# Kernel optimization log

Measured on AMD Instinct MI355X. Metric: run time of the kernel, lower is better.

## Reference

```python
import jax, jax.numpy as jnp
import numpy as np

N = 50000       # nodes
E = 800000      # edges (before self-loops)
G = 64          # graphs in batch
F_IN = 128      # node_features
HID = 64        # hidden_channels
H1 = 8          # conv1 heads
NEG_SLOPE = 0.2
EPS = 1e-16


def _gat_layer(x, src, dst, W, att_src, att_dst, bias, heads, out_ch, concat):
    """PyG GATConv (eval mode: dropout inactive). src/dst include self-loops.
    x: [N, F_in]; W: [F_in, heads*out_ch]; att_*: [heads, out_ch]; bias: [heads*out_ch] or [out_ch]."""
    n = x.shape[0]
    h = (x @ W).reshape(n, heads, out_ch)                 # [N,H,C]
    a_s = jnp.sum(h * att_src, axis=-1)                   # [N,H]
    a_d = jnp.sum(h * att_dst, axis=-1)                   # [N,H]
    e = jax.nn.leaky_relu(a_s[src] + a_d[dst], NEG_SLOPE)  # [Etot,H]
    # segment softmax over incoming edges of each destination node
    m = jax.ops.segment_max(e, dst, num_segments=n)       # [N,H]
    e = jnp.exp(e - m[dst])
    denom = jax.ops.segment_sum(e, dst, num_segments=n)   # [N,H]
    alpha = e / (denom[dst] + EPS)                        # [Etot,H]
    msg = h[src] * alpha[:, :, None]                      # [Etot,H,C]
    out = jax.ops.segment_sum(msg, dst, num_segments=n)   # [N,H,C]
    if concat:
        out = out.reshape(n, heads * out_ch)
    else:
        out = out.mean(axis=1)
    return out + bias


def setup_inputs() -> dict:
    key = jax.random.key(0)
    ks = jax.random.split(key, 14)
    x = jax.random.normal(ks[0], (N, F_IN), dtype=jnp.float32)
    edge_index = jax.random.randint(ks[1], (2, E), 0, N, dtype=jnp.int64)
    batch_index = jnp.sort(jax.random.randint(ks[2], (N,), 0, G, dtype=jnp.int64))
    s = 0.05
    return {
        "x": x,
        "edge_index": edge_index,
        "batch_index": batch_index,
        "W1": jax.random.normal(ks[3], (F_IN, H1 * HID), dtype=jnp.float32) * s,
        "att_src1": jax.random.normal(ks[4], (H1, HID), dtype=jnp.float32) * s,
        "att_dst1": jax.random.normal(ks[5], (H1, HID), dtype=jnp.float32) * s,
        "b1": jnp.zeros((H1 * HID,), dtype=jnp.float32),
        "W2": jax.random.normal(ks[6], (H1 * HID, HID), dtype=jnp.float32) * s,
        "att_src2": jax.random.normal(ks[7], (1, HID), dtype=jnp.float32) * s,
        "att_dst2": jax.random.normal(ks[8], (1, HID), dtype=jnp.float32) * s,
        "b2": jnp.zeros((HID,), dtype=jnp.float32),
        "lin_W": jax.random.normal(ks[9], (HID, 1), dtype=jnp.float32) * s,
        "lin_b": jnp.zeros((1,), dtype=jnp.float32),
    }


def reference(x, edge_index, batch_index, W1, att_src1, att_dst1, b1,
              W2, att_src2, att_dst2, b2, lin_W, lin_b):
    n = x.shape[0]
    loops = jnp.arange(n, dtype=edge_index.dtype)
    src = jnp.concatenate([edge_index[0], loops])
    dst = jnp.concatenate([edge_index[1], loops])
    # eval mode: F.dropout is identity
    h = jax.nn.elu(_gat_layer(x, src, dst, W1, att_src1, att_dst1, b1, H1, HID, True))
    h = _gat_layer(h, src, dst, W2, att_src2, att_dst2, b2, 1, HID, False)
    # global mean pool over graphs
    sums = jax.ops.segment_sum(h, batch_index, num_segments=G)          # [G,HID]
    cnt = jax.ops.segment_sum(jnp.ones((n,), h.dtype), batch_index, num_segments=G)
    pooled = sums / jnp.maximum(cnt, 1.0)[:, None]
    return pooled @ lin_W + lin_b                                       # [G,1]
```

## Files before the change

### kernel.cpp

```cpp
#include <hip/hip_runtime.h>
#include <math.h>

#define NN 50000
#define EE 800000
#define ET 850000
#define GG 64
#define MPAD 50048
#define NCAP 64
#define NROW 50016
#define CSRI (NROW * NCAP)
#define CSTRIDE 32

typedef __attribute__((ext_vector_type(8))) short bf16x8;
typedef __attribute__((ext_vector_type(4))) float f32x4;

__device__ __forceinline__ float lrelu(float v) { return v > 0.f ? v : 0.2f * v; }

__device__ __forceinline__ unsigned short f2bf(float f) {
  unsigned u = __float_as_uint(f);
  u += 0x7FFFu + ((u >> 16) & 1u);
  return (unsigned short)(u >> 16);
}
__device__ __forceinline__ unsigned pack2(float a, float b) {
  return (unsigned)f2bf(a) | ((unsigned)f2bf(b) << 16);
}
__device__ __forceinline__ void i8acc(uint2 u, float a, float* o) {
  o[0] += a * (float)((int)(u.x << 24) >> 24);
  o[1] += a * (float)((int)(u.x << 16) >> 24);
  o[2] += a * (float)((int)(u.x <<  8) >> 24);
  o[3] += a * (float)((int)u.x >> 24);
  o[4] += a * (float)((int)(u.y << 24) >> 24);
  o[5] += a * (float)((int)(u.y << 16) >> 24);
  o[6] += a * (float)((int)(u.y <<  8) >> 24);
  o[7] += a * (float)((int)u.y >> 24);
}

#define INIT_BLOCKS 1563
#define CVT_X_BLOCKS 3128
#define CVT_W_BLOCKS 256
#define V_BLOCKS 2
#define GSEG_BLOCKS 196
__global__ __launch_bounds__(256) void prep_kernel(const float* __restrict__ x,
                                                   const float* __restrict__ W1,
                                                   const float* __restrict__ W2,
                                                   const float* __restrict__ att_s2,
                                                   const float* __restrict__ att_d2,
                                                   const float* __restrict__ linW,
                                                   const int* __restrict__ batch,
                                                   unsigned short* __restrict__ xb,
                                                   unsigned short* __restrict__ W1T,
                                                   float* __restrict__ Vs,
                                                   float* __restrict__ Vd,
                                                   float* __restrict__ Vz,
                                                   int* __restrict__ gstart,
                                                   int* __restrict__ cursor,
                                                   unsigned short* __restrict__ csr) {
  int b = blockIdx.x;
  if (b < INIT_BLOCKS) {
    int i = b * 256 + threadIdx.x;
    if (i < CSRI / 8) {
      uint4 sf = {0xC350C350u, 0xC350C350u, 0xC350C350u, 0xC350C350u};
      ((uint4*)csr)[i] = sf;
    }
    if (i < NROW) cursor[i * CSTRIDE] = 0;
  } else if (b < INIT_BLOCKS + CVT_X_BLOCKS) {
    int i8 = (b - INIT_BLOCKS) * 256 + threadIdx.x;
    if (i8 >= MPAD * 128 / 8) return;
    size_t e0 = (size_t)i8 * 8;
    int row = (int)(e0 >> 7);
    uint4 o;
    if (row < NN) {
      float4 f0 = *(const float4*)(x + e0);
      float4 f1 = *(const float4*)(x + e0 + 4);
      o.x = pack2(f0.x, f0.y); o.y = pack2(f0.z, f0.w);
      o.z = pack2(f1.x, f1.y); o.w = pack2(f1.z, f1.w);
    } else {
      o.x = o.y = o.z = o.w = 0u;
    }
    *(uint4*)(xb + e0) = o;
  } else if (b < INIT_BLOCKS + CVT_X_BLOCKS + CVT_W_BLOCKS) {
    int i = (b - INIT_BLOCKS - CVT_X_BLOCKS) * 256 + threadIdx.x;
    int k = i >> 9, n = i & 511;
    W1T[n * 128 + k] = f2bf(W1[i]);
  } else if (b < INIT_BLOCKS + CVT_X_BLOCKS + CVT_W_BLOCKS + V_BLOCKS) {
    int k = (b - INIT_BLOCKS - CVT_X_BLOCKS - CVT_W_BLOCKS) * 256 + threadIdx.x;
    float vs = 0.f, vd = 0.f, vz = 0.f;
#pragma unroll 8
    for (int c = 0; c < 64; ++c) {
      float w = W2[k * 64 + c];
      vs += w * att_s2[c];
      vd += w * att_d2[c];
      vz += w * linW[c];
    }
    Vs[k] = vs; Vd[k] = vd; Vz[k] = vz;
  } else {
    int e = (b - INIT_BLOCKS - CVT_X_BLOCKS - CVT_W_BLOCKS - V_BLOCKS) * 256 + threadIdx.x;
    if (e < NN) {
      int bb = batch[e];
      if (e == 0) {
        for (int g = 0; g <= bb; ++g) gstart[g] = 0;
      } else {
        int pb = batch[e - 1];
        for (int g = pb + 1; g <= bb; ++g) gstart[g] = e;
      }
      if (e == NN - 1) {
        for (int g = bb + 1; g <= GG; ++g) gstart[g] = NN;
      }
    }
  }
}

#define GEMM_BLOCKS 3128
#define SCAT_BLOCKS 831
#define SCAT_STRIDE (SCAT_BLOCKS * 256)
__global__ __launch_bounds__(256) void gemm1_scatter(const unsigned short* __restrict__ xb,
                                                     const unsigned short* __restrict__ W1T,
                                                     const float* __restrict__ att_s,
                                                     const float* __restrict__ att_d,
                                                     unsigned char* __restrict__ h1i,
                                                     float2* __restrict__ asc,
                                                     float* __restrict__ ad1,
                                                     const int* __restrict__ ei,
                                                     int* __restrict__ cursor,
                                                     unsigned short* __restrict__ csr) {
  __shared__ unsigned char st8[2][64 * 72];
  const int idx = blockIdx.x;
  const bool is_scat = ((idx & 3) == 3) && ((idx >> 2) < SCAT_BLOCKS);
  if (is_scat) {
    int base = (idx >> 2) * 256 + threadIdx.x;
#pragma unroll
    for (int k = 0; k < 4; ++k) {
      int e = base + k * SCAT_STRIDE;
      if (e < ET) {
        int src = (e < EE) ? ei[e] : (e - EE);
        int dst = (e < EE) ? ei[EE + e] : (e - EE);
        int pos = atomicAdd(&cursor[dst * CSTRIDE], 1);
        if (pos < NCAP) csr[dst * NCAP + pos] = (unsigned short)src;
      }
    }
    return;
  }
  const int gi = idx - min((idx + 1) >> 2, SCAT_BLOCKS);

  const int t = threadIdx.x, w = t >> 6, l = t & 63;
  const int bm = (gi >> 2) * 64;
  const int ypair = gi & 3;
  const int m16 = l & 15, q = l >> 4;
  const int row = bm + w * 16 + m16;

  const bf16x8* Ap = (const bf16x8*)(xb + (size_t)row * 128 + q * 8);
  bf16x8 a0 = Ap[0], a1 = Ap[4], a2 = Ap[8], a3 = Ap[12];

  const int r2 = t >> 2, c16 = (t & 3) * 16;

#pragma unroll
  for (int hh = 0; hh < 2; ++hh) {
    const int h = ypair * 2 + hh;
    const bf16x8* Bp = (const bf16x8*)(W1T + (size_t)(h * 64 + m16) * 128 + q * 8);
    f32x4 acc[4] = {};
#pragma unroll
    for (int c = 0; c < 4; ++c) {
      acc[c] = __builtin_amdgcn_mfma_f32_16x16x32_bf16(a0, Bp[(size_t)c * 256 + 0],  acc[c], 0, 0, 0);
      acc[c] = __builtin_amdgcn_mfma_f32_16x16x32_bf16(a1, Bp[(size_t)c * 256 + 4],  acc[c], 0, 0, 0);
      acc[c] = __builtin_amdgcn_mfma_f32_16x16x32_bf16(a2, Bp[(size_t)c * 256 + 8],  acc[c], 0, 0, 0);
      acc[c] = __builtin_amdgcn_mfma_f32_16x16x32_bf16(a3, Bp[(size_t)c * 256 + 12], acc[c], 0, 0, 0);
    }

    float ps[4] = {0.f, 0.f, 0.f, 0.f}, pd[4] = {0.f, 0.f, 0.f, 0.f};
    float pm[4];
#pragma unroll
    for (int r = 0; r < 4; ++r)
      pm[r] = fmaxf(fmaxf(fabsf(acc[0][r]), fabsf(acc[1][r])),
                    fmaxf(fabsf(acc[2][r]), fabsf(acc[3][r])));
#pragma unroll
    for (int c = 0; c < 4; ++c) {
      float ws = att_s[h * 64 + m16 + 16 * c];
      float wd = att_d[h * 64 + m16 + 16 * c];
#pragma unroll
      for (int r = 0; r < 4; ++r) {
        ps[r] += acc[c][r] * ws;
        pd[r] += acc[c][r] * wd;
      }
    }
#pragma unroll
    for (int off = 1; off < 16; off <<= 1) {
#pragma unroll
      for (int r = 0; r < 4; ++r) {
        ps[r] += __shfl_xor(ps[r], off);
        pd[r] += __shfl_xor(pd[r], off);
        pm[r] = fmaxf(pm[r], __shfl_xor(pm[r], off));
      }
    }
    if (m16 == 0) {
#pragma unroll
      for (int r = 0; r < 4; ++r) {
        int rr = bm + w * 16 + q * 4 + r;
        float2 av;
        av.x = (rr < NN) ? ps[r] : -1e30f;
        av.y = pm[r] * (1.0f / 127.0f);
        asc[rr * 8 + h] = av;
        ad1[rr * 8 + h] = (rr < NN) ? pd[r] : 0.f;
      }
    }

    float invq[4];
#pragma unroll
    for (int r = 0; r < 4; ++r)
      invq[r] = 127.0f * __builtin_amdgcn_rcpf(fmaxf(pm[r], 1e-30f));
#pragma unroll
    for (int c = 0; c < 4; ++c)
#pragma unroll
      for (int r = 0; r < 4; ++r) {
        int qv = (int)__builtin_rintf(acc[c][r] * invq[r]);
        st8[hh][(w * 16 + q * 4 + r) * 72 + m16 + 16 * c] = (unsigned char)(qv & 0xFF);
      }
    __syncthreads();
    const unsigned* sp = (const unsigned*)(st8[hh] + r2 * 72 + c16);
    uint4 o4; o4.x = sp[0]; o4.y = sp[1]; o4.z = sp[2]; o4.w = sp[3];
    *(uint4*)(h1i + (size_t)(bm + r2) * 512 + h * 64 + c16) = o4;
  }
}

#define ISSUE8(K, U0, U1, U2, U3, U4, U5, U6, U7, ASV, SCV) do {             \
    uint4 cc;                                                                \
    cc.x = __shfl(cb.x, (K)); cc.y = __shfl(cb.y, (K));                      \
    cc.z = __shfl(cb.z, (K)); cc.w = __shfl(cb.w, (K));                      \
    unsigned pr = (slot_a & 4) ? ((slot_a & 2) ? cc.w : cc.z)                \
                               : ((slot_a & 2) ? cc.y : cc.x);               \
    int my_src = (slot_a & 1) ? (int)(pr >> 16) : (int)(pr & 0xFFFFu);       \
    float2 av = asc[my_src * 8 + ha];                                        \
    ASV = av.x; SCV = av.y;                                                  \
    int s0 = (int)(cc.x & 0xFFFFu), s1 = (int)(cc.x >> 16);                  \
    int s2 = (int)(cc.y & 0xFFFFu), s3 = (int)(cc.y >> 16);                  \
    int s4 = (int)(cc.z & 0xFFFFu), s5 = (int)(cc.z >> 16);                  \
    int s6 = (int)(cc.w & 0xFFFFu), s7 = (int)(cc.w >> 16);                  \
    U0 = *(const uint2*)(h1i + (size_t)s0 * 512 + lane * 8);                 \
    U1 = *(const uint2*)(h1i + (size_t)s1 * 512 + lane * 8);                 \
    U2 = *(const uint2*)(h1i + (size_t)s2 * 512 + lane * 8);                 \
    U3 = *(const uint2*)(h1i + (size_t)s3 * 512 + lane * 8);                 \
    U4 = *(const uint2*)(h1i + (size_t)s4 * 512 + lane * 8);                 \
    U5 = *(const uint2*)(h1i + (size_t)s5 * 512 + lane * 8);                 \
    U6 = *(const uint2*)(h1i + (size_t)s6 * 512 + lane * 8);                 \
    U7 = *(const uint2*)(h1i + (size_t)s7 * 512 + lane * 8);                 \
  } while (0)

#define PROC8(U0, U1, U2, U3, U4, U5, U6, U7, ASV, SCV) do {                 \
    float myal = __expf(lrelu((ASV) + adv_a));                               \
    float d8 = myal;                                                         \
    d8 += __shfl_xor(d8, 1); d8 += __shfl_xor(d8, 2); d8 += __shfl_xor(d8, 4);\
    den += d8;                                                               \
    float ac = myal * (SCV);                                                 \
    float a0 = __shfl(ac, hb + 0), a1 = __shfl(ac, hb + 1);                  \
    float a2 = __shfl(ac, hb + 2), a3 = __shfl(ac, hb + 3);                  \
    float a4 = __shfl(ac, hb + 4), a5 = __shfl(ac, hb + 5);                  \
    float a6 = __shfl(ac, hb + 6), a7 = __shfl(ac, hb + 7);                  \
    i8acc(U0, a0, o); i8acc(U1, a1, o);                                      \
    i8acc(U2, a2, o); i8acc(U3, a3, o);                                      \
    i8acc(U4, a4, o); i8acc(U5, a5, o);                                      \
    i8acc(U6, a6, o); i8acc(U7, a7, o);                                      \
  } while (0)

__global__ __launch_bounds__(256) void agg1_kernel(const unsigned char* __restrict__ h1i,
                                                   const float2* __restrict__ asc,
                                                   const float* __restrict__ ad1,
                                                   const int* __restrict__ cnt,
                                                   const unsigned short* __restrict__ csr,
                                                   const float* __restrict__ b1,
                                                   const float* __restrict__ Vs,
                                                   const float* __restrict__ Vd,
                                                   const float* __restrict__ Vz,
                                                   float* __restrict__ as2,
                                                   float* __restrict__ ad2,
                                                   float* __restrict__ zz) {
  int dst = blockIdx.x * 4 + (threadIdx.x >> 6);
  int lane = threadIdx.x & 63;
  if (dst >= NN) return;
  const int ha = lane >> 3;
  const int hb = ha * 8;
  const int slot_a = lane & 7;

  const int cv = min(cnt[dst * CSTRIDE], NCAP);
  const uint4 cb = *(const uint4*)(csr + dst * NCAP + (lane & 7) * 8);
  const float adv_a = ad1[dst * 8 + ha];
  const int nb = (cv + 7) >> 3;

  float den = 0.f;
  float o[8] = {0.f, 0.f, 0.f, 0.f, 0.f, 0.f, 0.f, 0.f};
  uint2 A0, A1, A2, A3, A4, A5, A6, A7;
  uint2 B0, B1, B2, B3, B4, B5, B6, B7;
  float asA, asB, scA, scB;

  ISSUE8(0, A0, A1, A2, A3, A4, A5, A6, A7, asA, scA);
  int k = 0;
  for (;;) {
    if (k + 1 < nb) ISSUE8(k + 1, B0, B1, B2, B3, B4, B5, B6, B7, asB, scB);
    PROC8(A0, A1, A2, A3, A4, A5, A6, A7, asA, scA);
    if (++k >= nb) break;
    if (k + 1 < nb) ISSUE8(k + 1, A0, A1, A2, A3, A4, A5, A6, A7, asA, scA);
    PROC8(B0, B1, B2, B3, B4, B5, B6, B7, asB, scB);
    if (++k >= nb) break;
  }
  float inv = 1.0f / (den + 1e-16f);

  const float4* bp = (const float4*)(b1 + lane * 8);
  float4 bb0 = bp[0], bb1 = bp[1];
  float bb[8] = {bb0.x, bb0.y, bb0.z, bb0.w, bb1.x, bb1.y, bb1.z, bb1.w};
  float v[8];
#pragma unroll
  for (int j = 0; j < 8; ++j) {
    float t = o[j] * inv + bb[j];
    v[j] = (t > 0.f) ? t : (__expf(t) - 1.0f);
  }

  const float4* vsp = (const float4*)(Vs + lane * 8);
  const float4* vdp = (const float4*)(Vd + lane * 8);
  const float4* vzp = (const float4*)(Vz + lane * 8);
  float4 vs0 = vsp[0], vs1 = vsp[1];
  float4 vd0 = vdp[0], vd1 = vdp[1];
  float4 vz0 = vzp[0], vz1 = vzp[1];
  float ps = v[0]*vs0.x + v[1]*vs0.y + v[2]*vs0.z + v[3]*vs0.w
           + v[4]*vs1.x + v[5]*vs1.y + v[6]*vs1.z + v[7]*vs1.w;
  float pd = v[0]*vd0.x + v[1]*vd0.y + v[2]*vd0.z + v[3]*vd0.w
           + v[4]*vd1.x + v[5]*vd1.y + v[6]*vd1.z + v[7]*vd1.w;
  float pz = v[0]*vz0.x + v[1]*vz0.y + v[2]*vz0.z + v[3]*vz0.w
           + v[4]*vz1.x + v[5]*vz1.y + v[6]*vz1.z + v[7]*vz1.w;
#pragma unroll
  for (int off = 1; off < 64; off <<= 1) {
    ps += __shfl_xor(ps, off);
    pd += __shfl_xor(pd, off);
    pz += __shfl_xor(pz, off);
  }
  if (lane == 0) {
    as2[dst] = ps;
    ad2[dst] = pd;
    zz[dst]  = pz;
  }
}

__global__ __launch_bounds__(256) void agg2z_kernel(const float* __restrict__ as2,
                                                    const float* __restrict__ ad2,
                                                    const float* __restrict__ z,
                                                    const int* __restrict__ cnt,
                                                    const unsigned short* __restrict__ csr,
                                                    float* __restrict__ s) {
  int dst = blockIdx.x * 4 + (threadIdx.x >> 6);
  int lane = threadIdx.x & 63;
  if (dst >= NN) return;
  const int si = dst * NCAP, e = si + cnt[dst * CSTRIDE];
  const float adv = ad2[dst];
  float num = 0.f, den = 0.f;
  for (int i = si + lane; i < e; i += 64) {
    int src = csr[i];
    float a = __expf(lrelu(as2[src] + adv));
    num += a * z[src];
    den += a;
  }
#pragma unroll
  for (int off = 32; off > 0; off >>= 1) {
    num += __shfl_xor(num, off);
    den += __shfl_xor(den, off);
  }
  if (lane == 0) s[dst] = num / (den + 1e-16f);
}

__global__ __launch_bounds__(256) void poolz_kernel(const float* __restrict__ s,
                                                    const int* __restrict__ gstart,
                                                    const float* __restrict__ b2,
                                                    const float* __restrict__ linW,
                                                    const float* __restrict__ linb,
                                                    float* __restrict__ out) {
  __shared__ float red[4];
  int g = blockIdx.x;
  int t = threadIdx.x, lane = t & 63, w = t >> 6;
  int s0 = gstart[g], e0 = gstart[g + 1];
  float acc = 0.f;
  for (int i = s0 + t; i < e0; i += 256) acc += s[i];
#pragma unroll
  for (int off = 32; off > 0; off >>= 1) acc += __shfl_xor(acc, off);
  if (lane == 0) red[w] = acc;
  __syncthreads();
  if (w == 0) {
    float total = red[0] + red[1] + red[2] + red[3];
    float bz = b2[lane] * linW[lane];
#pragma unroll
    for (int off = 32; off > 0; off >>= 1) bz += __shfl_xor(bz, off);
    if (lane == 0) {
      float cnt = fmaxf((float)(e0 - s0), 1.0f);
      out[g] = total / cnt + bz + linb[0];
    }
  }
}

extern "C" void kernel_launch(void* const* d_in, const int* in_sizes, int n_in,
                              void* d_out, int out_size, void* d_ws, size_t ws_size,
                              hipStream_t stream) {
  const float* x      = (const float*)d_in[0];
  const int*   ei     = (const int*)d_in[1];
  const int*   batch  = (const int*)d_in[2];
  const float* W1     = (const float*)d_in[3];
  const float* att_s1 = (const float*)d_in[4];
  const float* att_d1 = (const float*)d_in[5];
  const float* b1     = (const float*)d_in[6];
  const float* W2     = (const float*)d_in[7];
  const float* att_s2 = (const float*)d_in[8];
  const float* att_d2 = (const float*)d_in[9];
  const float* b2     = (const float*)d_in[10];
  const float* linW   = (const float*)d_in[11];
  const float* linb   = (const float*)d_in[12];
  float* out = (float*)d_out;

  char* base = (char*)d_ws;
  unsigned short* xb  = (unsigned short*)base; base += (size_t)MPAD * 128 * 2;
  unsigned char*  h1i = (unsigned char*)base;  base += (size_t)MPAD * 512;
  unsigned short* W1T = (unsigned short*)base; base += (size_t)512 * 128 * 2;
  float* Vs   = (float*)base; base += (size_t)512 * 4;
  float* Vd   = (float*)base; base += (size_t)512 * 4;
  float* Vz   = (float*)base; base += (size_t)512 * 4;
  float2* asc = (float2*)base; base += (size_t)MPAD * 8 * 8;
  float* ad1  = (float*)base; base += (size_t)MPAD * 8 * 4;
  float* as2  = (float*)base; base += (size_t)NROW * 4;
  float* ad2  = (float*)base; base += (size_t)NROW * 4;
  float* zz   = (float*)base; base += (size_t)NROW * 4;
  float* sv   = (float*)base; base += (size_t)NROW * 4;
  int* cursor = (int*)base;  base += (size_t)NROW * CSTRIDE * 4;
  unsigned short* csr = (unsigned short*)base; base += (size_t)CSRI * 2;
  int* gstart = (int*)base;  base += (size_t)(GG + 16) * 4;

  if (ws_size < (size_t)(base - (char*)d_ws)) return;

  prep_kernel<<<INIT_BLOCKS + CVT_X_BLOCKS + CVT_W_BLOCKS + V_BLOCKS + GSEG_BLOCKS,
                256, 0, stream>>>(x, W1, W2, att_s2, att_d2, linW, batch,
                                  xb, W1T, Vs, Vd, Vz, gstart, cursor, csr);

  gemm1_scatter<<<GEMM_BLOCKS + SCAT_BLOCKS, 256, 0, stream>>>(
      xb, W1T, att_s1, att_d1, h1i, asc, ad1, ei, cursor, csr);

  agg1_kernel<<<12500, 256, 0, stream>>>(h1i, asc, ad1, cursor, csr, b1,
                                         Vs, Vd, Vz, as2, ad2, zz);

  agg2z_kernel<<<12500, 256, 0, stream>>>(as2, ad2, zz, cursor, csr, sv);
  poolz_kernel<<<GG, 256, 0, stream>>>(sv, gstart, b2, linW, linb, out);
}
```

Baseline: 264.7 us.

## Split layer-1 aggregation per head with dst-range scatter and head-major scores

Edge scatter moves into the prep kernel and is partitioned by destination range, so each block only inserts edges whose dst falls in one of eight ranges. The cursor array becomes dense, and a separate init kernel clears it. Attention scores are stored head-major. The layer-1 aggregation now runs one block per (head, group of 16 destinations): each lane gathers 8 int8 channels of one head, and per-head partial projections are written out and then summed by a new reduction kernel. The aim is better locality for the scatter atomics and gathers, at the cost of reading the edge list eight times, more launches, and extra partial-sum traffic.

```diff
diff --git a/kernel.cpp b/kernel.cpp
--- a/kernel.cpp
+++ b/kernel.cpp
@@ -9,7 +9,7 @@
 #define NCAP 64
 #define NROW 50016
 #define CSRI (NROW * NCAP)
-#define CSTRIDE 32
+#define DRANGE 6250
 
 typedef __attribute__((ext_vector_type(8))) short bf16x8;
 typedef __attribute__((ext_vector_type(4))) float f32x4;
@@ -36,6 +36,17 @@
 }
 
 #define INIT_BLOCKS 1563
+__global__ __launch_bounds__(256) void init_kernel(unsigned short* __restrict__ csr,
+                                                   int* __restrict__ cursor) {
+  int i = blockIdx.x * 256 + threadIdx.x;
+  if (i < CSRI / 8) {
+    uint4 sf = {0xC350C350u, 0xC350C350u, 0xC350C350u, 0xC350C350u};
+    ((uint4*)csr)[i] = sf;
+  }
+  if (i < NROW) cursor[i] = 0;
+}
+
+#define SCATB 3328
 #define CVT_X_BLOCKS 3128
 #define CVT_W_BLOCKS 256
 #define V_BLOCKS 2
@@ -47,6 +58,7 @@
                                                    const float* __restrict__ att_d2,
                                                    const float* __restrict__ linW,
                                                    const int* __restrict__ batch,
+                                                   const int* __restrict__ ei,
                                                    unsigned short* __restrict__ xb,
                                                    unsigned short* __restrict__ W1T,
                                                    float* __restrict__ Vs,
@@ -56,15 +68,26 @@
                                                    int* __restrict__ cursor,
                                                    unsigned short* __restrict__ csr) {
   int b = blockIdx.x;
-  if (b < INIT_BLOCKS) {
-    int i = b * 256 + threadIdx.x;
-    if (i < CSRI / 8) {
-      uint4 sf = {0xC350C350u, 0xC350C350u, 0xC350C350u, 0xC350C350u};
-      ((uint4*)csr)[i] = sf;
-    }
-    if (i < NROW) cursor[i * CSTRIDE] = 0;
-  } else if (b < INIT_BLOCKS + CVT_X_BLOCKS) {
-    int i8 = (b - INIT_BLOCKS) * 256 + threadIdx.x;
+  if (b < SCATB) {
+    const unsigned lo = (unsigned)((b & 7) * DRANGE);
+    const int base = (b >> 3) * 2048 + threadIdx.x;
+#pragma unroll
+    for (int j = 0; j < 8; ++j) {
+      int e = base + j * 256;
+      if (e < ET) {
+        int dst = (e < EE) ? ei[EE + e] : (e - EE);
+        if ((unsigned)dst - lo < (unsigned)DRANGE) {
+          int src = (e < EE) ? ei[e] : (e - EE);
+          int pos = atomicAdd(&cursor[dst], 1);
+          if (pos < NCAP) csr[(size_t)dst * NCAP + pos] = (unsigned short)src;
+        }
+      }
+    }
+    return;
+  }
+  int c = b - SCATB;
+  if (c < CVT_X_BLOCKS) {
+    int i8 = c * 256 + threadIdx.x;
     if (i8 >= MPAD * 128 / 8) return;
     size_t e0 = (size_t)i8 * 8;
     int row = (int)(e0 >> 7);
@@ -78,23 +101,23 @@
       o.x = o.y = o.z = o.w = 0u;
     }
     *(uint4*)(xb + e0) = o;
-  } else if (b < INIT_BLOCKS + CVT_X_BLOCKS + CVT_W_BLOCKS) {
-    int i = (b - INIT_BLOCKS - CVT_X_BLOCKS) * 256 + threadIdx.x;
+  } else if (c < CVT_X_BLOCKS + CVT_W_BLOCKS) {
+    int i = (c - CVT_X_BLOCKS) * 256 + threadIdx.x;
     int k = i >> 9, n = i & 511;
     W1T[n * 128 + k] = f2bf(W1[i]);
-  } else if (b < INIT_BLOCKS + CVT_X_BLOCKS + CVT_W_BLOCKS + V_BLOCKS) {
-    int k = (b - INIT_BLOCKS - CVT_X_BLOCKS - CVT_W_BLOCKS) * 256 + threadIdx.x;
+  } else if (c < CVT_X_BLOCKS + CVT_W_BLOCKS + V_BLOCKS) {
+    int k = (c - CVT_X_BLOCKS - CVT_W_BLOCKS) * 256 + threadIdx.x;
     float vs = 0.f, vd = 0.f, vz = 0.f;
 #pragma unroll 8
-    for (int c = 0; c < 64; ++c) {
-      float w = W2[k * 64 + c];
-      vs += w * att_s2[c];
-      vd += w * att_d2[c];
-      vz += w * linW[c];
+    for (int cc = 0; cc < 64; ++cc) {
+      float w = W2[k * 64 + cc];
+      vs += w * att_s2[cc];
+      vd += w * att_d2[cc];
+      vz += w * linW[cc];
     }
     Vs[k] = vs; Vd[k] = vd; Vz[k] = vz;
   } else {
-    int e = (b - INIT_BLOCKS - CVT_X_BLOCKS - CVT_W_BLOCKS - V_BLOCKS) * 256 + threadIdx.x;
+    int e = (c - CVT_X_BLOCKS - CVT_W_BLOCKS - V_BLOCKS) * 256 + threadIdx.x;
     if (e < NN) {
       int bb = batch[e];
       if (e == 0) {
@@ -111,36 +134,15 @@
 }
 
 #define GEMM_BLOCKS 3128
-#define SCAT_BLOCKS 831
-#define SCAT_STRIDE (SCAT_BLOCKS * 256)
-__global__ __launch_bounds__(256) void gemm1_scatter(const unsigned short* __restrict__ xb,
-                                                     const unsigned short* __restrict__ W1T,
-                                                     const float* __restrict__ att_s,
-                                                     const float* __restrict__ att_d,
-                                                     unsigned char* __restrict__ h1i,
-                                                     float2* __restrict__ asc,
-                                                     float* __restrict__ ad1,
-                                                     const int* __restrict__ ei,
-                                                     int* __restrict__ cursor,
-                                                     unsigned short* __restrict__ csr) {
+__global__ __launch_bounds__(256) void gemm1_kernel(const unsigned short* __restrict__ xb,
+                                                    const unsigned short* __restrict__ W1T,
+                                                    const float* __restrict__ att_s,
+                                                    const float* __restrict__ att_d,
+                                                    unsigned char* __restrict__ h1i,
+                                                    float2* __restrict__ asc,
+                                                    float* __restrict__ ad1) {
   __shared__ unsigned char st8[2][64 * 72];
-  const int idx = blockIdx.x;
-  const bool is_scat = ((idx & 3) == 3) && ((idx >> 2) < SCAT_BLOCKS);
-  if (is_scat) {
-    int base = (idx >> 2) * 256 + threadIdx.x;
-#pragma unroll
-    for (int k = 0; k < 4; ++k) {
-      int e = base + k * SCAT_STRIDE;
-      if (e < ET) {
-        int src = (e < EE) ? ei[e] : (e - EE);
-        int dst = (e < EE) ? ei[EE + e] : (e - EE);
-        int pos = atomicAdd(&cursor[dst * CSTRIDE], 1);
-        if (pos < NCAP) csr[dst * NCAP + pos] = (unsigned short)src;
-      }
-    }
-    return;
-  }
-  const int gi = idx - min((idx + 1) >> 2, SCAT_BLOCKS);
+  const int gi = blockIdx.x;
 
   const int t = threadIdx.x, w = t >> 6, l = t & 63;
   const int bm = (gi >> 2) * 64;
@@ -198,8 +200,8 @@
         float2 av;
         av.x = (rr < NN) ? ps[r] : -1e30f;
         av.y = pm[r] * (1.0f / 127.0f);
-        asc[rr * 8 + h] = av;
-        ad1[rr * 8 + h] = (rr < NN) ? pd[r] : 0.f;
+        asc[(size_t)h * MPAD + rr] = av;
+        ad1[(size_t)h * MPAD + rr] = (rr < NN) ? pd[r] : 0.f;
       }
     }
 
@@ -221,43 +223,20 @@
   }
 }
 
-#define ISSUE8(K, U0, U1, U2, U3, U4, U5, U6, U7, ASV, SCV) do {             \
-    uint4 cc;                                                                \
-    cc.x = __shfl(cb.x, (K)); cc.y = __shfl(cb.y, (K));                      \
-    cc.z = __shfl(cb.z, (K)); cc.w = __shfl(cb.w, (K));                      \
-    unsigned pr = (slot_a & 4) ? ((slot_a & 2) ? cc.w : cc.z)                \
-                               : ((slot_a & 2) ? cc.y : cc.x);               \
-    int my_src = (slot_a & 1) ? (int)(pr >> 16) : (int)(pr & 0xFFFFu);       \
-    float2 av = asc[my_src * 8 + ha];                                        \
-    ASV = av.x; SCV = av.y;                                                  \
-    int s0 = (int)(cc.x & 0xFFFFu), s1 = (int)(cc.x >> 16);                  \
-    int s2 = (int)(cc.y & 0xFFFFu), s3 = (int)(cc.y >> 16);                  \
-    int s4 = (int)(cc.z & 0xFFFFu), s5 = (int)(cc.z >> 16);                  \
-    int s6 = (int)(cc.w & 0xFFFFu), s7 = (int)(cc.w >> 16);                  \
-    U0 = *(const uint2*)(h1i + (size_t)s0 * 512 + lane * 8);                 \
-    U1 = *(const uint2*)(h1i + (size_t)s1 * 512 + lane * 8);                 \
-    U2 = *(const uint2*)(h1i + (size_t)s2 * 512 + lane * 8);                 \
-    U3 = *(const uint2*)(h1i + (size_t)s3 * 512 + lane * 8);                 \
-    U4 = *(const uint2*)(h1i + (size_t)s4 * 512 + lane * 8);                 \
-    U5 = *(const uint2*)(h1i + (size_t)s5 * 512 + lane * 8);                 \
-    U6 = *(const uint2*)(h1i + (size_t)s6 * 512 + lane * 8);                 \
-    U7 = *(const uint2*)(h1i + (size_t)s7 * 512 + lane * 8);                 \
+#define ISS(K, UU, AA) do {                                                  \
+    unsigned c0 = __shfl(cb.x, (K)), c1 = __shfl(cb.y, (K));                 \
+    unsigned c2 = __shfl(cb.z, (K)), c3 = __shfl(cb.w, (K));                 \
+    unsigned pr = (slot & 4) ? ((slot & 2) ? c3 : c2)                        \
+                             : ((slot & 2) ? c1 : c0);                       \
+    int ms = (slot & 1) ? (int)(pr >> 16) : (int)(pr & 0xFFFFu);             \
+    AA = ascH[ms];                                                           \
+    UU = *(const uint2*)(h1g + (size_t)ms * 512);                            \
   } while (0)
 
-#define PROC8(U0, U1, U2, U3, U4, U5, U6, U7, ASV, SCV) do {                 \
-    float myal = __expf(lrelu((ASV) + adv_a));                               \
-    float d8 = myal;                                                         \
-    d8 += __shfl_xor(d8, 1); d8 += __shfl_xor(d8, 2); d8 += __shfl_xor(d8, 4);\
-    den += d8;                                                               \
-    float ac = myal * (SCV);                                                 \
-    float a0 = __shfl(ac, hb + 0), a1 = __shfl(ac, hb + 1);                  \
-    float a2 = __shfl(ac, hb + 2), a3 = __shfl(ac, hb + 3);                  \
-    float a4 = __shfl(ac, hb + 4), a5 = __shfl(ac, hb + 5);                  \
-    float a6 = __shfl(ac, hb + 6), a7 = __shfl(ac, hb + 7);                  \
-    i8acc(U0, a0, o); i8acc(U1, a1, o);                                      \
-    i8acc(U2, a2, o); i8acc(U3, a3, o);                                      \
-    i8acc(U4, a4, o); i8acc(U5, a5, o);                                      \
-    i8acc(U6, a6, o); i8acc(U7, a7, o);                                      \
+#define PRC(UU, AA) do {                                                     \
+    float myal = __expf(lrelu(AA.x + adv));                                  \
+    den += myal;                                                             \
+    i8acc(UU, myal * AA.y, o);                                               \
   } while (0)
 
 __global__ __launch_bounds__(256) void agg1_kernel(const unsigned char* __restrict__ h1i,
@@ -269,72 +248,103 @@
                                                    const float* __restrict__ Vs,
                                                    const float* __restrict__ Vd,
                                                    const float* __restrict__ Vz,
+                                                   float* __restrict__ ppS,
+                                                   float* __restrict__ ppD,
+                                                   float* __restrict__ ppZ) {
+  const int head = blockIdx.x & 7;
+  const int gg = blockIdx.x >> 3;
+  const int wv = threadIdx.x >> 6, lane = threadIdx.x & 63;
+  const int slot = lane >> 3, cg = lane & 7;
+  const int coff = head * 64 + cg * 8;
+
+  const float2* ascH = asc + (size_t)head * MPAD;
+  const float*  adH  = ad1 + (size_t)head * MPAD;
+  const unsigned char* h1g = h1i + coff;
+
+  const float4* bp  = (const float4*)(b1 + coff);
+  const float4* vsp = (const float4*)(Vs + coff);
+  const float4* vdp = (const float4*)(Vd + coff);
+  const float4* vzp = (const float4*)(Vz + coff);
+  float4 bb0 = bp[0],  bb1 = bp[1];
+  float4 vs0 = vsp[0], vs1 = vsp[1];
+  float4 vd0 = vdp[0], vd1 = vdp[1];
+  float4 vz0 = vzp[0], vz1 = vzp[1];
+  float bb[8] = {bb0.x, bb0.y, bb0.z, bb0.w, bb1.x, bb1.y, bb1.z, bb1.w};
+
+  const int dbase = gg * 16 + wv * 4;
+#pragma unroll 1
+  for (int di = 0; di < 4; ++di) {
+    int dst = dbase + di;
+    if (dst >= NN) break;
+    const int cv = min(cnt[dst], NCAP);
+    const int nb = (cv + 7) >> 3;
+    uint4 cb = {0u, 0u, 0u, 0u};
+    if (lane < 8 && lane * 8 < cv)
+      cb = *(const uint4*)(csr + (size_t)dst * NCAP + lane * 8);
+    const float adv = adH[dst];
+
+    float den = 0.f;
+    float o[8] = {0.f, 0.f, 0.f, 0.f, 0.f, 0.f, 0.f, 0.f};
+    uint2 Ua, Ub; float2 Aa, Ab;
+    ISS(0, Ua, Aa);
+    int k = 0;
+    for (;;) {
+      if (k + 1 < nb) ISS(k + 1, Ub, Ab);
+      PRC(Ua, Aa);
+      if (++k >= nb) break;
+      if (k + 1 < nb) ISS(k + 1, Ua, Aa);
+      PRC(Ub, Ab);
+      if (++k >= nb) break;
+    }
+
+    den += __shfl_xor(den, 8); den += __shfl_xor(den, 16); den += __shfl_xor(den, 32);
+#pragma unroll
+    for (int j = 0; j < 8; ++j) {
+      o[j] += __shfl_xor(o[j], 8);
+      o[j] += __shfl_xor(o[j], 16);
+      o[j] += __shfl_xor(o[j], 32);
+    }
+    float inv = 1.0f / (den + 1e-16f);
+
+    float v[8];
+#pragma unroll
+    for (int j = 0; j < 8; ++j) {
+      float tt = o[j] * inv + bb[j];
+      v[j] = (tt > 0.f) ? tt : (__expf(tt) - 1.0f);
+    }
+    float ps = v[0]*vs0.x + v[1]*vs0.y + v[2]*vs0.z + v[3]*vs0.w
+             + v[4]*vs1.x + v[5]*vs1.y + v[6]*vs1.z + v[7]*vs1.w;
+    float pd = v[0]*vd0.x + v[1]*vd0.y + v[2]*vd0.z + v[3]*vd0.w
+             + v[4]*vd1.x + v[5]*vd1.y + v[6]*vd1.z + v[7]*vd1.w;
+    float pz = v[0]*vz0.x + v[1]*vz0.y + v[2]*vz0.z + v[3]*vz0.w
+             + v[4]*vz1.x + v[5]*vz1.y + v[6]*vz1.z + v[7]*vz1.w;
+    ps += __shfl_xor(ps, 1); ps += __shfl_xor(ps, 2); ps += __shfl_xor(ps, 4);
+    pd += __shfl_xor(pd, 1); pd += __shfl_xor(pd, 2); pd += __shfl_xor(pd, 4);
+    pz += __shfl_xor(pz, 1); pz += __shfl_xor(pz, 2); pz += __shfl_xor(pz, 4);
+    if (lane == 0) {
+      ppS[(size_t)head * NROW + dst] = ps;
+      ppD[(size_t)head * NROW + dst] = pd;
+      ppZ[(size_t)head * NROW + dst] = pz;
+    }
+  }
+}
+
+__global__ __launch_bounds__(256) void redu_kernel(const float* __restrict__ ppS,
+                                                   const float* __restrict__ ppD,
+                                                   const float* __restrict__ ppZ,
                                                    float* __restrict__ as2,
                                                    float* __restrict__ ad2,
                                                    float* __restrict__ zz) {
-  int dst = blockIdx.x * 4 + (threadIdx.x >> 6);
-  int lane = threadIdx.x & 63;
-  if (dst >= NN) return;
-  const int ha = lane >> 3;
-  const int hb = ha * 8;
-  const int slot_a = lane & 7;
-
-  const int cv = min(cnt[dst * CSTRIDE], NCAP);
-  const uint4 cb = *(const uint4*)(csr + dst * NCAP + (lane & 7) * 8);
-  const float adv_a = ad1[dst * 8 + ha];
-  const int nb = (cv + 7) >> 3;
-
-  float den = 0.f;
-  float o[8] = {0.f, 0.f, 0.f, 0.f, 0.f, 0.f, 0.f, 0.f};
-  uint2 A0, A1, A2, A3, A4, A5, A6, A7;
-  uint2 B0, B1, B2, B3, B4, B5, B6, B7;
-  float asA, asB, scA, scB;
-
-  ISSUE8(0, A0, A1, A2, A3, A4, A5, A6, A7, asA, scA);
-  int k = 0;
-  for (;;) {
-    if (k + 1 < nb) ISSUE8(k + 1, B0, B1, B2, B3, B4, B5, B6, B7, asB, scB);
-    PROC8(A0, A1, A2, A3, A4, A5, A6, A7, asA, scA);
-    if (++k >= nb) break;
-    if (k + 1 < nb) ISSUE8(k + 1, A0, A1, A2, A3, A4, A5, A6, A7, asA, scA);
-    PROC8(B0, B1, B2, B3, B4, B5, B6, B7, asB, scB);
-    if (++k >= nb) break;
-  }
-  float inv = 1.0f / (den + 1e-16f);
-
-  const float4* bp = (const float4*)(b1 + lane * 8);
-  float4 bb0 = bp[0], bb1 = bp[1];
-  float bb[8] = {bb0.x, bb0.y, bb0.z, bb0.w, bb1.x, bb1.y, bb1.z, bb1.w};
-  float v[8];
-#pragma unroll
-  for (int j = 0; j < 8; ++j) {
-    float t = o[j] * inv + bb[j];
-    v[j] = (t > 0.f) ? t : (__expf(t) - 1.0f);
-  }
-
-  const float4* vsp = (const float4*)(Vs + lane * 8);
-  const float4* vdp = (const float4*)(Vd + lane * 8);
-  const float4* vzp = (const float4*)(Vz + lane * 8);
-  float4 vs0 = vsp[0], vs1 = vsp[1];
-  float4 vd0 = vdp[0], vd1 = vdp[1];
-  float4 vz0 = vzp[0], vz1 = vzp[1];
-  float ps = v[0]*vs0.x + v[1]*vs0.y + v[2]*vs0.z + v[3]*vs0.w
-           + v[4]*vs1.x + v[5]*vs1.y + v[6]*vs1.z + v[7]*vs1.w;
-  float pd = v[0]*vd0.x + v[1]*vd0.y + v[2]*vd0.z + v[3]*vd0.w
-           + v[4]*vd1.x + v[5]*vd1.y + v[6]*vd1.z + v[7]*vd1.w;
-  float pz = v[0]*vz0.x + v[1]*vz0.y + v[2]*vz0.z + v[3]*vz0.w
-           + v[4]*vz1.x + v[5]*vz1.y + v[6]*vz1.z + v[7]*vz1.w;
-#pragma unroll
-  for (int off = 1; off < 64; off <<= 1) {
-    ps += __shfl_xor(ps, off);
-    pd += __shfl_xor(pd, off);
-    pz += __shfl_xor(pz, off);
-  }
-  if (lane == 0) {
-    as2[dst] = ps;
-    ad2[dst] = pd;
-    zz[dst]  = pz;
-  }
+  int i = blockIdx.x * 256 + threadIdx.x;
+  if (i >= NN) return;
+  float s = 0.f, d = 0.f, z = 0.f;
+#pragma unroll
+  for (int h = 0; h < 8; ++h) {
+    s += ppS[(size_t)h * NROW + i];
+    d += ppD[(size_t)h * NROW + i];
+    z += ppZ[(size_t)h * NROW + i];
+  }
+  as2[i] = s; ad2[i] = d; zz[i] = z;
 }
 
 __global__ __launch_bounds__(256) void agg2z_kernel(const float* __restrict__ as2,
@@ -346,7 +356,7 @@
   int dst = blockIdx.x * 4 + (threadIdx.x >> 6);
   int lane = threadIdx.x & 63;
   if (dst >= NN) return;
-  const int si = dst * NCAP, e = si + cnt[dst * CSTRIDE];
+  const int si = dst * NCAP, e = si + min(cnt[dst], NCAP);
   const float adv = ad2[dst];
   float num = 0.f, den = 0.f;
   for (int i = si + lane; i < e; i += 64) {
@@ -416,27 +426,33 @@
   float* Vs   = (float*)base; base += (size_t)512 * 4;
   float* Vd   = (float*)base; base += (size_t)512 * 4;
   float* Vz   = (float*)base; base += (size_t)512 * 4;
-  float2* asc = (float2*)base; base += (size_t)MPAD * 8 * 8;
-  float* ad1  = (float*)base; base += (size_t)MPAD * 8 * 4;
+  float2* asc = (float2*)base; base += (size_t)8 * MPAD * 8;
+  float* ad1  = (float*)base; base += (size_t)8 * MPAD * 4;
+  float* ppS  = (float*)base; base += (size_t)8 * NROW * 4;
+  float* ppD  = (float*)base; base += (size_t)8 * NROW * 4;
+  float* ppZ  = (float*)base; base += (size_t)8 * NROW * 4;
   float* as2  = (float*)base; base += (size_t)NROW * 4;
   float* ad2  = (float*)base; base += (size_t)NROW * 4;
   float* zz   = (float*)base; base += (size_t)NROW * 4;
   float* sv   = (float*)base; base += (size_t)NROW * 4;
-  int* cursor = (int*)base;  base += (size_t)NROW * CSTRIDE * 4;
+  int* cursor = (int*)base;  base += (size_t)NROW * 4;
   unsigned short* csr = (unsigned short*)base; base += (size_t)CSRI * 2;
   int* gstart = (int*)base;  base += (size_t)(GG + 16) * 4;
 
   if (ws_size < (size_t)(base - (char*)d_ws)) return;
 
-  prep_kernel<<<INIT_BLOCKS + CVT_X_BLOCKS + CVT_W_BLOCKS + V_BLOCKS + GSEG_BLOCKS,
-                256, 0, stream>>>(x, W1, W2, att_s2, att_d2, linW, batch,
+  init_kernel<<<INIT_BLOCKS, 256, 0, stream>>>(csr, cursor);
+
+  prep_kernel<<<SCATB + CVT_X_BLOCKS + CVT_W_BLOCKS + V_BLOCKS + GSEG_BLOCKS,
+                256, 0, stream>>>(x, W1, W2, att_s2, att_d2, linW, batch, ei,
                                   xb, W1T, Vs, Vd, Vz, gstart, cursor, csr);
 
-  gemm1_scatter<<<GEMM_BLOCKS + SCAT_BLOCKS, 256, 0, stream>>>(
-      xb, W1T, att_s1, att_d1, h1i, asc, ad1, ei, cursor, csr);
-
-  agg1_kernel<<<12500, 256, 0, stream>>>(h1i, asc, ad1, cursor, csr, b1,
-                                         Vs, Vd, Vz, as2, ad2, zz);
+  gemm1_kernel<<<GEMM_BLOCKS, 256, 0, stream>>>(xb, W1T, att_s1, att_d1,
+                                                h1i, asc, ad1);
+
+  agg1_kernel<<<8 * 3125, 256, 0, stream>>>(h1i, asc, ad1, cursor, csr, b1,
+                                            Vs, Vd, Vz, ppS, ppD, ppZ);
+  redu_kernel<<<196, 256, 0, stream>>>(ppS, ppD, ppZ, as2, ad2, zz);
 
   agg2z_kernel<<<12500, 256, 0, stream>>>(as2, ad2, zz, cursor, csr, sv);
   poolz_kernel<<<GG, 256, 0, stream>>>(sv, gstart, b2, linW, linb, out);
```

Measured after the change: 417.0 us. +57.5%, slower.

## Build CSR via per-block dst-range scans with shared-memory cursors instead of global atomics

Applied to the files above, without the earlier changes.

Replaces the global-atomic edge scatter with 128 blocks that each own a range of 391 destination nodes. Each block scans the whole dst array and uses shared-memory atomics to place its edges. Self-loops are pre-seeded into slot 0 during CSR init, and the padded per-node cursor array becomes a dense count array. This removes contended global atomics and the strided cursor memory, but every scan block rereads all 800K dst indices, so total read traffic grows roughly 128-fold.

```diff
diff --git a/kernel.cpp b/kernel.cpp
--- a/kernel.cpp
+++ b/kernel.cpp
@@ -9,7 +9,6 @@
 #define NCAP 64
 #define NROW 50016
 #define CSRI (NROW * NCAP)
-#define CSTRIDE 32
 
 typedef __attribute__((ext_vector_type(8))) short bf16x8;
 typedef __attribute__((ext_vector_type(4))) float f32x4;
@@ -53,16 +52,15 @@
                                                    float* __restrict__ Vd,
                                                    float* __restrict__ Vz,
                                                    int* __restrict__ gstart,
-                                                   int* __restrict__ cursor,
                                                    unsigned short* __restrict__ csr) {
   int b = blockIdx.x;
   if (b < INIT_BLOCKS) {
     int i = b * 256 + threadIdx.x;
     if (i < CSRI / 8) {
       uint4 sf = {0xC350C350u, 0xC350C350u, 0xC350C350u, 0xC350C350u};
+      if ((i & 7) == 0) sf.x = 0xC3500000u | (unsigned)(i >> 3);
       ((uint4*)csr)[i] = sf;
     }
-    if (i < NROW) cursor[i * CSTRIDE] = 0;
   } else if (b < INIT_BLOCKS + CVT_X_BLOCKS) {
     int i8 = (b - INIT_BLOCKS) * 256 + threadIdx.x;
     if (i8 >= MPAD * 128 / 8) return;
@@ -110,37 +108,52 @@
   }
 }
 
+#define SCANB 128
+#define DR 391
 #define GEMM_BLOCKS 3128
-#define SCAT_BLOCKS 831
-#define SCAT_STRIDE (SCAT_BLOCKS * 256)
-__global__ __launch_bounds__(256) void gemm1_scatter(const unsigned short* __restrict__ xb,
-                                                     const unsigned short* __restrict__ W1T,
-                                                     const float* __restrict__ att_s,
-                                                     const float* __restrict__ att_d,
-                                                     unsigned char* __restrict__ h1i,
-                                                     float2* __restrict__ asc,
-                                                     float* __restrict__ ad1,
-                                                     const int* __restrict__ ei,
-                                                     int* __restrict__ cursor,
-                                                     unsigned short* __restrict__ csr) {
+__global__ __launch_bounds__(256) void gemm1_scan(const unsigned short* __restrict__ xb,
+                                                  const unsigned short* __restrict__ W1T,
+                                                  const float* __restrict__ att_s,
+                                                  const float* __restrict__ att_d,
+                                                  unsigned char* __restrict__ h1i,
+                                                  float2* __restrict__ asc,
+                                                  float* __restrict__ ad1,
+                                                  const int* __restrict__ ei,
+                                                  int* __restrict__ cursor,
+                                                  unsigned short* __restrict__ csr) {
+  const int idx = blockIdx.x;
+  if (idx < SCANB) {
+    __shared__ int lcur[DR];
+    const int lo = idx * DR;
+    for (int j = threadIdx.x; j < DR; j += 256) lcur[j] = 1;
+    __syncthreads();
+    const uint4* di4 = (const uint4*)(ei + EE);
+    for (int it = 0; it < 782; ++it) {
+      int i4 = it * 256 + threadIdx.x;
+      if (i4 < EE / 4) {
+        uint4 dv = di4[i4];
+        int e0 = i4 * 4;
+        int dd[4] = {(int)dv.x, (int)dv.y, (int)dv.z, (int)dv.w};
+#pragma unroll
+        for (int j = 0; j < 4; ++j) {
+          if ((unsigned)(dd[j] - lo) < (unsigned)DR) {
+            int pos = atomicAdd(&lcur[dd[j] - lo], 1);
+            if (pos < NCAP)
+              csr[(size_t)dd[j] * NCAP + pos] = (unsigned short)ei[e0 + j];
+          }
+        }
+      }
+    }
+    __syncthreads();
+    for (int j = threadIdx.x; j < DR; j += 256) {
+      int d = lo + j;
+      if (d < NN) cursor[d] = lcur[j];
+    }
+    return;
+  }
+
   __shared__ unsigned char st8[2][64 * 72];
-  const int idx = blockIdx.x;
-  const bool is_scat = ((idx & 3) == 3) && ((idx >> 2) < SCAT_BLOCKS);
-  if (is_scat) {
-    int base = (idx >> 2) * 256 + threadIdx.x;
-#pragma unroll
-    for (int k = 0; k < 4; ++k) {
-      int e = base + k * SCAT_STRIDE;
-      if (e < ET) {
-        int src = (e < EE) ? ei[e] : (e - EE);
-        int dst = (e < EE) ? ei[EE + e] : (e - EE);
-        int pos = atomicAdd(&cursor[dst * CSTRIDE], 1);
-        if (pos < NCAP) csr[dst * NCAP + pos] = (unsigned short)src;
-      }
-    }
-    return;
-  }
-  const int gi = idx - min((idx + 1) >> 2, SCAT_BLOCKS);
+  const int gi = idx - SCANB;
 
   const int t = threadIdx.x, w = t >> 6, l = t & 63;
   const int bm = (gi >> 2) * 64;
@@ -279,8 +292,8 @@
   const int hb = ha * 8;
   const int slot_a = lane & 7;
 
-  const int cv = min(cnt[dst * CSTRIDE], NCAP);
-  const uint4 cb = *(const uint4*)(csr + dst * NCAP + (lane & 7) * 8);
+  const int cv = min(cnt[dst], NCAP);
+  const uint4 cb = *(const uint4*)(csr + (size_t)dst * NCAP + (lane & 7) * 8);
   const float adv_a = ad1[dst * 8 + ha];
   const int nb = (cv + 7) >> 3;
 
@@ -346,7 +359,7 @@
   int dst = blockIdx.x * 4 + (threadIdx.x >> 6);
   int lane = threadIdx.x & 63;
   if (dst >= NN) return;
-  const int si = dst * NCAP, e = si + cnt[dst * CSTRIDE];
+  const int si = dst * NCAP, e = si + min(cnt[dst], NCAP);
   const float adv = ad2[dst];
   float num = 0.f, den = 0.f;
   for (int i = si + lane; i < e; i += 64) {
@@ -422,7 +435,7 @@
   float* ad2  = (float*)base; base += (size_t)NROW * 4;
   float* zz   = (float*)base; base += (size_t)NROW * 4;
   float* sv   = (float*)base; base += (size_t)NROW * 4;
-  int* cursor = (int*)base;  base += (size_t)NROW * CSTRIDE * 4;
+  int* cursor = (int*)base;  base += (size_t)NROW * 4;
   unsigned short* csr = (unsigned short*)base; base += (size_t)CSRI * 2;
   int* gstart = (int*)base;  base += (size_t)(GG + 16) * 4;
 
@@ -430,9 +443,9 @@
 
   prep_kernel<<<INIT_BLOCKS + CVT_X_BLOCKS + CVT_W_BLOCKS + V_BLOCKS + GSEG_BLOCKS,
                 256, 0, stream>>>(x, W1, W2, att_s2, att_d2, linW, batch,
-                                  xb, W1T, Vs, Vd, Vz, gstart, cursor, csr);
-
-  gemm1_scatter<<<GEMM_BLOCKS + SCAT_BLOCKS, 256, 0, stream>>>(
+                                  xb, W1T, Vs, Vd, Vz, gstart, csr);
+
+  gemm1_scan<<<SCANB + GEMM_BLOCKS, 256, 0, stream>>>(
       xb, W1T, att_s1, att_d1, h1i, asc, ad1, ei, cursor, csr);
 
   agg1_kernel<<<12500, 256, 0, stream>>>(h1i, asc, ad1, cursor, csr, b1,
```

Result: slower. 682.4 us (+157.8%).

## Deepen agg1 gather prefetch, pack as2/z, and unpad cursor counters

Applied to the files above, without the earlier changes.

The agg1 neighbor loop moves from double to triple buffering, so two batches of 8 neighbor rows are in flight while one is processed. This hides more gather latency but raises register pressure. The per-node layer-2 scalars as2 and z are packed into one float2 array, so agg2 does one 8-byte gather per neighbor instead of two loads. The cursor counters lose their 32-int padding, which shrinks init and lookup footprint but may add atomic contention on shared cache lines during the scatter.

```diff
diff --git a/kernel.cpp b/kernel.cpp
--- a/kernel.cpp
+++ b/kernel.cpp
@@ -9,7 +9,6 @@
 #define NCAP 64
 #define NROW 50016
 #define CSRI (NROW * NCAP)
-#define CSTRIDE 32
 
 typedef __attribute__((ext_vector_type(8))) short bf16x8;
 typedef __attribute__((ext_vector_type(4))) float f32x4;
@@ -62,7 +61,7 @@
       uint4 sf = {0xC350C350u, 0xC350C350u, 0xC350C350u, 0xC350C350u};
       ((uint4*)csr)[i] = sf;
     }
-    if (i < NROW) cursor[i * CSTRIDE] = 0;
+    if (i < NROW) cursor[i] = 0;
   } else if (b < INIT_BLOCKS + CVT_X_BLOCKS) {
     int i8 = (b - INIT_BLOCKS) * 256 + threadIdx.x;
     if (i8 >= MPAD * 128 / 8) return;
@@ -134,8 +133,8 @@
       if (e < ET) {
         int src = (e < EE) ? ei[e] : (e - EE);
         int dst = (e < EE) ? ei[EE + e] : (e - EE);
-        int pos = atomicAdd(&cursor[dst * CSTRIDE], 1);
-        if (pos < NCAP) csr[dst * NCAP + pos] = (unsigned short)src;
+        int pos = atomicAdd(&cursor[dst], 1);
+        if (pos < NCAP) csr[(size_t)dst * NCAP + pos] = (unsigned short)src;
       }
     }
     return;
@@ -269,9 +268,8 @@
                                                    const float* __restrict__ Vs,
                                                    const float* __restrict__ Vd,
                                                    const float* __restrict__ Vz,
-                                                   float* __restrict__ as2,
-                                                   float* __restrict__ ad2,
-                                                   float* __restrict__ zz) {
+                                                   float2* __restrict__ azz,
+                                                   float* __restrict__ ad2) {
   int dst = blockIdx.x * 4 + (threadIdx.x >> 6);
   int lane = threadIdx.x & 63;
   if (dst >= NN) return;
@@ -279,8 +277,8 @@
   const int hb = ha * 8;
   const int slot_a = lane & 7;
 
-  const int cv = min(cnt[dst * CSTRIDE], NCAP);
-  const uint4 cb = *(const uint4*)(csr + dst * NCAP + (lane & 7) * 8);
+  const int cv = min(cnt[dst], NCAP);
+  const uint4 cb = *(const uint4*)(csr + (size_t)dst * NCAP + (lane & 7) * 8);
   const float adv_a = ad1[dst * 8 + ha];
   const int nb = (cv + 7) >> 3;
 
@@ -288,16 +286,21 @@
   float o[8] = {0.f, 0.f, 0.f, 0.f, 0.f, 0.f, 0.f, 0.f};
   uint2 A0, A1, A2, A3, A4, A5, A6, A7;
   uint2 B0, B1, B2, B3, B4, B5, B6, B7;
-  float asA, asB, scA, scB;
+  uint2 C0, C1, C2, C3, C4, C5, C6, C7;
+  float asA, asB, asC, scA, scB, scC;
 
   ISSUE8(0, A0, A1, A2, A3, A4, A5, A6, A7, asA, scA);
+  if (nb > 1) ISSUE8(1, B0, B1, B2, B3, B4, B5, B6, B7, asB, scB);
   int k = 0;
   for (;;) {
-    if (k + 1 < nb) ISSUE8(k + 1, B0, B1, B2, B3, B4, B5, B6, B7, asB, scB);
+    if (k + 2 < nb) ISSUE8(k + 2, C0, C1, C2, C3, C4, C5, C6, C7, asC, scC);
     PROC8(A0, A1, A2, A3, A4, A5, A6, A7, asA, scA);
     if (++k >= nb) break;
-    if (k + 1 < nb) ISSUE8(k + 1, A0, A1, A2, A3, A4, A5, A6, A7, asA, scA);
+    if (k + 2 < nb) ISSUE8(k + 2, A0, A1, A2, A3, A4, A5, A6, A7, asA, scA);
     PROC8(B0, B1, B2, B3, B4, B5, B6, B7, asB, scB);
+    if (++k >= nb) break;
+    if (k + 2 < nb) ISSUE8(k + 2, B0, B1, B2, B3, B4, B5, B6, B7, asB, scB);
+    PROC8(C0, C1, C2, C3, C4, C5, C6, C7, asC, scC);
     if (++k >= nb) break;
   }
   float inv = 1.0f / (den + 1e-16f);
@@ -331,28 +334,28 @@
     pz += __shfl_xor(pz, off);
   }
   if (lane == 0) {
-    as2[dst] = ps;
+    float2 az; az.x = ps; az.y = pz;
+    azz[dst] = az;
     ad2[dst] = pd;
-    zz[dst]  = pz;
-  }
-}
-
-__global__ __launch_bounds__(256) void agg2z_kernel(const float* __restrict__ as2,
+  }
+}
+
+__global__ __launch_bounds__(256) void agg2z_kernel(const float2* __restrict__ azz,
                                                     const float* __restrict__ ad2,
-                                                    const float* __restrict__ z,
                                                     const int* __restrict__ cnt,
                                                     const unsigned short* __restrict__ csr,
                                                     float* __restrict__ s) {
   int dst = blockIdx.x * 4 + (threadIdx.x >> 6);
   int lane = threadIdx.x & 63;
   if (dst >= NN) return;
-  const int si = dst * NCAP, e = si + cnt[dst * CSTRIDE];
+  const int si = dst * NCAP, e = si + min(cnt[dst], NCAP);
   const float adv = ad2[dst];
   float num = 0.f, den = 0.f;
   for (int i = si + lane; i < e; i += 64) {
     int src = csr[i];
-    float a = __expf(lrelu(as2[src] + adv));
-    num += a * z[src];
+    float2 az = azz[src];
+    float a = __expf(lrelu(az.x + adv));
+    num += a * az.y;
     den += a;
   }
 #pragma unroll
@@ -418,11 +421,10 @@
   float* Vz   = (float*)base; base += (size_t)512 * 4;
   float2* asc = (float2*)base; base += (size_t)MPAD * 8 * 8;
   float* ad1  = (float*)base; base += (size_t)MPAD * 8 * 4;
-  float* as2  = (float*)base; base += (size_t)NROW * 4;
+  float2* azz = (float2*)base; base += (size_t)NROW * 8;
   float* ad2  = (float*)base; base += (size_t)NROW * 4;
-  float* zz   = (float*)base; base += (size_t)NROW * 4;
   float* sv   = (float*)base; base += (size_t)NROW * 4;
-  int* cursor = (int*)base;  base += (size_t)NROW * CSTRIDE * 4;
+  int* cursor = (int*)base;  base += (size_t)NROW * 4;
   unsigned short* csr = (unsigned short*)base; base += (size_t)CSRI * 2;
   int* gstart = (int*)base;  base += (size_t)(GG + 16) * 4;
 
@@ -436,8 +438,8 @@
       xb, W1T, att_s1, att_d1, h1i, asc, ad1, ei, cursor, csr);
 
   agg1_kernel<<<12500, 256, 0, stream>>>(h1i, asc, ad1, cursor, csr, b1,
-                                         Vs, Vd, Vz, as2, ad2, zz);
-
-  agg2z_kernel<<<12500, 256, 0, stream>>>(as2, ad2, zz, cursor, csr, sv);
+                                         Vs, Vd, Vz, azz, ad2);
+
+  agg2z_kernel<<<12500, 256, 0, stream>>>(azz, ad2, cursor, csr, sv);
   poolz_kernel<<<GG, 256, 0, stream>>>(sv, gstart, b2, linW, linb, out);
 }
```

New measurement: 284.5 us. 7.5% more time.
